# Kernel optimization log

Measured on AMD Instinct MI355X. Metric: run time of the kernel, lower is better.

The kernel has to match this reference:

```python
import jax, jax.numpy as jnp
import numpy as np

K, B, T, Y, X, HY, HX = 8, 64, 128, 128, 64, 256, 256


def sparsemax(z):
    # projection onto the simplex along last axis
    zs = jnp.flip(jnp.sort(z, axis=-1), axis=-1)
    k = jnp.arange(1, z.shape[-1] + 1, dtype=z.dtype)
    cssv = jnp.cumsum(zs, axis=-1) - 1.0
    cond = k * zs > cssv
    kz = jnp.sum(cond, axis=-1, keepdims=True)
    tau = jnp.take_along_axis(cssv, kz - 1, axis=-1) / kz.astype(z.dtype)
    return jnp.maximum(z - tau, 0.0)


def rnn_relu(x, Wih, Whh, bih, bhh, h0):
    # batch-first relu RNN: x [B,T,D] -> h [B,T,H]
    xW = jnp.einsum('btd,hd->bth', x, Wih) + bih
    h0b = jnp.broadcast_to(h0, (x.shape[0], h0.shape[0]))
    def step(h, xt):
        h = jax.nn.relu(xt + h @ Whh.T + bhh)
        return h, h
    _, hs = jax.lax.scan(step, h0b, jnp.swapaxes(xW, 0, 1))
    return jnp.swapaxes(hs, 0, 1)


def setup_inputs() -> dict:
    ks = jax.random.split(jax.random.key(0), 32)
    s = 0.05
    p = lambda k, sh: jax.random.normal(k, sh, jnp.float32) * s
    return {
        'data': jax.random.normal(ks[0], (B, T, Y), jnp.float32),
        'eps_qx': jax.random.normal(ks[1], (K, B, T, X), jnp.float32),
        'eps_z': jax.random.normal(ks[2], (T, B, K), jnp.float32),
        'eps_x': jax.random.normal(ks[3], (T, B, X), jnp.float32),
        'y_Wih': p(ks[4], (K, HY, Y)), 'y_Whh': p(ks[5], (K, HY, HY)),
        'y_bih': p(ks[6], (K, HY)), 'y_bhh': p(ks[7], (K, HY)),
        'y_h0': jnp.zeros((K, HY), jnp.float32),
        'y_Wmu': p(ks[8], (K, X, HY)), 'y_bmu': p(ks[9], (K, X)),
        'x_Wih': p(ks[10], (K, HX, X)), 'x_Whh': p(ks[11], (K, HX, HX)),
        'x_bih': p(ks[12], (K, HX)), 'x_bhh': p(ks[13], (K, HX)),
        'x_h0': jnp.zeros((K, HX), jnp.float32),
        'ds_W': p(ks[14], (HX, K * HX)), 'ds_b': p(ks[15], (HX,)),
        'cb_W1': p(ks[16], (HX, K)), 'cb_b1': p(ks[17], (HX,)),
        'cb_W2': p(ks[18], (K, HX)), 'cb_b2': p(ks[19], (K,)),
        'z_q0': jnp.zeros((K,), jnp.float32),
    }


def _forward(data, eps_qx, eps_z, eps_x, y_Wih, y_Whh, y_bih, y_bhh, y_h0,
             y_Wmu, y_bmu, x_Wih, x_Whh, x_bih, x_bhh, x_h0,
             ds_W, ds_b, cb_W1, cb_b1, cb_W2, cb_b2, z_q0):
    Bn, Tn, _ = data.shape
    Kn = z_q0.shape[0]
    vr = jax.vmap(rnn_relu, in_axes=(None, 0, 0, 0, 0, 0))
    vrx = jax.vmap(rnn_relu, in_axes=(0, 0, 0, 0, 0, 0))
    # per-state LDM inference over reversed y: q(x^k_{1:T} | y_{1:T})
    data_rev = jnp.flip(data, axis=1)
    h_y = jnp.flip(vr(data_rev, y_Wih, y_Whh, y_bih, y_bhh, y_h0), axis=2)  # [K,B,T,HY]
    q_x_mu = jnp.einsum('kbth,kxh->kbtx', h_y, y_Wmu) + y_bmu[:, None, None, :]
    q_x_logvar = jnp.zeros_like(q_x_mu)
    q_x = q_x_mu + eps_qx  # sigma = exp(0.5*0) = 1
    # per-state summary RNN over reversed q_x samples
    q_x_rev = jnp.flip(q_x, axis=2)
    h_x = jnp.flip(vrx(q_x_rev, x_Wih, x_Whh, x_bih, x_bhh, x_h0), axis=2)  # [K,B,T,HX]
    summary = jnp.transpose(h_x, (1, 2, 0, 3)).reshape(Bn, Tn, -1)  # [B,T,K*HX]
    xs = summary @ ds_W.T + ds_b  # downsampler -> [B,T,HX]
    xs_t_all = jnp.swapaxes(xs, 0, 1)              # [T,B,HX]
    mu_t_all = jnp.transpose(q_x_mu, (2, 1, 0, 3))  # [T,B,K,X]
    z0 = jnp.broadcast_to(z_q0, (Bn, Kn))
    def step(z_prev, inp):
        xs_t, mu_t, ez, ex = inp
        h = z_prev @ cb_W1.T + cb_b1 + xs_t          # combiner hidden
        z_mu = h @ cb_W2.T + cb_b2                   # logits mu (logvar=0)
        z_t = z_mu + ez
        w = sparsemax(z_t)                            # [B,K] gating
        x_t = jnp.einsum('bk,bkx->bx', w, mu_t) + ex  # mixture reparam (sigma=1)
        return z_t, (x_t, z_t, z_mu)
    _, (x_s, z_s, z_l) = jax.lax.scan(step, z0, (xs_t_all, mu_t_all, eps_z, eps_x))
    x_sample = jnp.swapaxes(x_s, 0, 1)
    z_sample = jnp.swapaxes(z_s, 0, 1)
    z_logits = jnp.swapaxes(z_l, 0, 1)
    return (x_sample, q_x_mu, q_x_logvar, z_sample, z_logits)


def reference(data, eps_qx, eps_z, eps_x, y_Wih, y_Whh, y_bih, y_bhh, y_h0,
              y_Wmu, y_bmu, x_Wih, x_Whh, x_bih, x_bhh, x_h0,
              ds_W, ds_b, cb_W1, cb_b1, cb_W2, cb_b2, z_q0):
    return _forward(data, eps_qx, eps_z, eps_x, y_Wih, y_Whh, y_bih, y_bhh, y_h0,
                    y_Wmu, y_bmu, x_Wih, x_Whh, x_bih, x_bhh, x_h0,
                    ds_W, ds_b, cb_W1, cb_b1, cb_W2, cb_b2, z_q0)
```

## Files before the change

kernel.cpp:

```cpp
#include <hip/hip_runtime.h>

#define Kc 8
#define Bc 64
#define Tc 128
#define Yc 128
#define Xc 64
#define Hc 256
#define Rc 8192

typedef unsigned short u16;
typedef unsigned int u32;
typedef __attribute__((ext_vector_type(8))) short short8;
typedef __attribute__((ext_vector_type(4))) float f32x4;
typedef __attribute__((ext_vector_type(2))) unsigned int u32x2;

#define OFF_DATA 0L
#define OFF_YWIH 1048576L
#define OFF_YWHH 1310720L
#define OFF_YWMU 1835008L
#define OFF_XWIH 1966080L
#define OFF_XWHH 2097152L
#define OFF_M2   2621440L
#define OFF_QXF  2654208L
#define OFF_BUF1 6848512L
#define U16_BYTES 80805888L
#define FO_YB 0L
#define FO_XB 2048L
#define FO_CB 4096L
#define FO_A2 4112L
#define FO_CP 8192L
#define FO_C  532480L
#define FO_W  598016L


#define O_XS  0L
#define O_QMU 524288L
#define O_QLV 4718592L
#define O_ZS  8912896L
#define O_ZL  8978432L

__device__ __forceinline__ u16 f2bf(float f) {
  union { float f; u32 u; } v; v.f = f;
  u32 u = v.u;
  return (u16)((u + 0x7FFFu + ((u >> 16) & 1u)) >> 16);
}
__device__ __forceinline__ float bitsf(u32 u) {
  union { u32 u; float f; } v; v.u = u; return v.f;
}
__device__ __forceinline__ u32 cvt_pk(float lo, float hi) {
  u32 r;
  asm("v_cvt_pk_bf16_f32 %0, %1, %2" : "=v"(r) : "v"(lo), "v"(hi));
  return r;
}
__device__ __forceinline__ f32x4 mfma16(short8 a, short8 b, f32x4 c) {
  return __builtin_amdgcn_mfma_f32_16x16x32_bf16(a, b, c, 0, 0, 0);
}

__global__ void k_prep(const float* __restrict__ data, const float* __restrict__ yWih,
                       const float* __restrict__ yWhh, const float* __restrict__ yWmu,
                       const float* __restrict__ xWih, const float* __restrict__ xWhh,
                       const float* __restrict__ ybih, const float* __restrict__ ybhh,
                       const float* __restrict__ xbih, const float* __restrict__ xbhh,
                       u16* __restrict__ W, float* __restrict__ F, float* __restrict__ out)
{
  long tid = (long)blockIdx.x * blockDim.x + threadIdx.x;
  long stride = (long)gridDim.x * blockDim.x;
  for (long i = tid; i < 1048576L; i += stride) W[OFF_DATA + i] = f2bf(data[i]);
  for (long i = tid; i < 262144L;  i += stride) W[OFF_YWIH + i] = f2bf(yWih[i]);
  for (long i = tid; i < 524288L;  i += stride) W[OFF_YWHH + i] = f2bf(yWhh[i]);
  for (long i = tid; i < 131072L;  i += stride) W[OFF_YWMU + i] = f2bf(yWmu[i]);
  for (long i = tid; i < 131072L;  i += stride) W[OFF_XWIH + i] = f2bf(xWih[i]);
  for (long i = tid; i < 524288L;  i += stride) W[OFF_XWHH + i] = f2bf(xWhh[i]);
  for (long i = tid; i < 2048L;    i += stride) F[FO_YB + i] = ybih[i] + ybhh[i];
  for (long i = tid; i < 2048L;    i += stride) F[FO_XB + i] = xbih[i] + xbhh[i];
  for (long i = tid; i < 4194304L; i += stride) out[O_QLV + i] = 0.0f;
}

__global__ void k_prep2(const float* __restrict__ dsW, const float* __restrict__ dsb,
                        const float* __restrict__ W1, const float* __restrict__ b1,
                        const float* __restrict__ W2, const float* __restrict__ b2,
                        u16* __restrict__ W, float* __restrict__ F)
{
  if (blockIdx.x < 128) {
    long i = (long)blockIdx.x * 256 + threadIdx.x;
    int k2 = (int)(i >> 11), ki = (int)(i & 2047);
    float s = 0.0f;
    if (k2 < 8) {
      for (int j = 0; j < 256; ++j) s += W2[k2 * 256 + j] * dsW[(long)j * 2048 + ki];
    }
    W[OFF_M2 + i] = f2bf(s);
  } else {
    int t = threadIdx.x;
    if (t < 64) {
      int k2 = t >> 3, k1 = t & 7;
      float s = 0.0f;
      for (int j = 0; j < 256; ++j) s += W2[k2 * 256 + j] * W1[j * 8 + k1];
      F[FO_A2 + t] = s;
    } else if (t < 80) {
      int k2 = t - 64;
      float s = 0.0f;
      if (k2 < 8) {
        for (int j = 0; j < 256; ++j) s += W2[k2 * 256 + j] * (dsb[j] + b1[j]);
        s += b2[k2];
      }
      F[FO_CB + k2] = s;
    }
  }
}

__global__ __launch_bounds__(256) void k_g1(const u16* __restrict__ W, const float* __restrict__ F,
                                            u16* __restrict__ buf)
{
  const int k = blockIdx.y, bs = blockIdx.x >> 5, t0 = (blockIdx.x & 31) * 4;
  const int tid = threadIdx.x, wv = tid >> 6, l = tid & 63, lr = l & 15, lk = l >> 4;
  const int b0 = bs * 16;
  short8 Af[4][4];
  const u16* Ak = W + OFF_YWIH + (long)k * 32768;
#pragma unroll
  for (int nt = 0; nt < 4; ++nt)
#pragma unroll
    for (int kk = 0; kk < 4; ++kk)
      Af[nt][kk] = *(const short8*)(Ak + (long)(wv * 64 + nt * 16 + lr) * 128 + kk * 32 + lk * 8);
  f32x4 bias[4];
#pragma unroll
  for (int nt = 0; nt < 4; ++nt)
    bias[nt] = *(const f32x4*)&F[FO_YB + k * 256 + wv * 64 + nt * 16 + lk * 4];
  int roff[4];
#pragma unroll
  for (int nt = 0; nt < 4; ++nt)
    roff[nt] = (wv * 2 + (nt >> 1)) * 512 + ((nt & 1) * 2 + (lk >> 1)) * 128 + lr * 8 + (lk & 1) * 4;

  for (int ti = 0; ti < 4; ++ti) {
    int t = t0 + ti;
    f32x4 acc[4] = {bias[0], bias[1], bias[2], bias[3]};
    const u16* Brow = W + OFF_DATA + ((long)(b0 + lr) * 128 + t) * 128 + lk * 8;
#pragma unroll
    for (int kk = 0; kk < 4; ++kk) {
      short8 b = *(const short8*)(Brow + kk * 32);
      acc[0] = mfma16(Af[0][kk], b, acc[0]);
      acc[1] = mfma16(Af[1][kk], b, acc[1]);
      acc[2] = mfma16(Af[2][kk], b, acc[2]);
      acc[3] = mfma16(Af[3][kk], b, acc[3]);
    }
    u16* tb = buf + ((long)(k * 4 + bs) * 128 + t) * 4096;
#pragma unroll
    for (int nt = 0; nt < 4; ++nt) {
      u32 d0 = cvt_pk(acc[nt][0], acc[nt][1]);
      u32 d1 = cvt_pk(acc[nt][2], acc[nt][3]);
      *(u32x2*)(tb + roff[nt]) = (u32x2){d0, d1};
    }
  }
}

#define RNNY_STEP(T_, XW_, PIN_, POUT_)                                       \
  {                                                                           \
    f32x4 acc0, acc1;                                                         \
    { u32 w0 = XW_[0], w1 = XW_[1];                                           \
      acc0[0] = bitsf(w0 << 16); acc0[1] = bitsf(w0 & 0xffff0000u);           \
      acc0[2] = bitsf(w1 << 16); acc0[3] = bitsf(w1 & 0xffff0000u); }         \
    { u32 w0 = XW_[2], w1 = XW_[3];                                           \
      acc1[0] = bitsf(w0 << 16); acc1[1] = bitsf(w0 & 0xffff0000u);           \
      acc1[2] = bitsf(w1 << 16); acc1[3] = bitsf(w1 & 0xffff0000u); }         \
    if ((T_) >= 2) {                                                          \
      u32x2 v0 = *(const u32x2*)(tb0 + (long)((T_) - 2) * 4096 + roff[0]);    \
      u32x2 v1 = *(const u32x2*)(tb0 + (long)((T_) - 2) * 4096 + roff[1]);    \
      XW_[0] = v0.x; XW_[1] = v0.y; XW_[2] = v1.x; XW_[3] = v1.y;             \
    }                                                                         \
    _Pragma("unroll")                                                         \
    for (int kk = 0; kk < 8; ++kk) {                                          \
      short8 b = *(const short8*)&hlds[PIN_][kk * 512 + fro];                 \
      acc0 = mfma16(Bf[0][kk], b, acc0);                                      \
      acc1 = mfma16(Bf[1][kk], b, acc1);                                      \
    }                                                                         \
    u16* tb = tb0 + (long)(T_) * 4096;                                        \
    { u32x2 d = (u32x2){cvt_pk(fmaxf(acc0[0], 0.f), fmaxf(acc0[1], 0.f)),     \
                        cvt_pk(fmaxf(acc0[2], 0.f), fmaxf(acc0[3], 0.f))};    \
      *(u32x2*)&hlds[POUT_][roff[0]] = d; *(u32x2*)(tb + roff[0]) = d; }      \
    { u32x2 d = (u32x2){cvt_pk(fmaxf(acc1[0], 0.f), fmaxf(acc1[1], 0.f)),     \
                        cvt_pk(fmaxf(acc1[2], 0.f), fmaxf(acc1[3], 0.f))};    \
      *(u32x2*)&hlds[POUT_][roff[1]] = d; *(u32x2*)(tb + roff[1]) = d; }      \
    asm volatile("s_waitcnt lgkmcnt(0)" ::: "memory");                        \
    __builtin_amdgcn_s_barrier();                                             \
    __builtin_amdgcn_sched_barrier(0);                                        \
  }

__global__ __launch_bounds__(512, 1) void k_rnnY(u16* __restrict__ buf,
                                                 const u16* __restrict__ Whh,
                                                 const float* __restrict__ h0)
{
  const int k = blockIdx.y, bs = blockIdx.x;
  const int tid = threadIdx.x, wv = tid >> 6, l = tid & 63, lr = l & 15, lk = l >> 4;
  const int fro = lk * 128 + lr * 8;
  __shared__ __align__(16) u16 hlds[2][4096];

  short8 Bf[2][8];
  const u16* Wk = Whh + (long)k * 65536;
#pragma unroll
  for (int nt = 0; nt < 2; ++nt)
#pragma unroll
    for (int kk = 0; kk < 8; ++kk)
      Bf[nt][kk] = *(const short8*)(Wk + (long)(wv * 32 + nt * 16 + lr) * 256 + kk * 32 + lk * 8);

  for (int i = tid; i < 4096; i += 512) {
    int n = (i >> 9) * 32 + ((i >> 7) & 3) * 8 + (i & 7);
    hlds[0][i] = f2bf(h0[k * 256 + n]);
  }

  u16* tb0 = buf + (long)(k * 4 + bs) * 128 * 4096;
  int roff[2];
#pragma unroll
  for (int nt = 0; nt < 2; ++nt)
    roff[nt] = wv * 512 + (nt * 2 + (lk >> 1)) * 128 + lr * 8 + (lk & 1) * 4;

  u32 xwA[4], xwB[4];
  {
    u32x2 a0 = *(const u32x2*)(tb0 + (long)(Tc - 1) * 4096 + roff[0]);
    u32x2 a1 = *(const u32x2*)(tb0 + (long)(Tc - 1) * 4096 + roff[1]);
    xwA[0] = a0.x; xwA[1] = a0.y; xwA[2] = a1.x; xwA[3] = a1.y;
    u32x2 b0v = *(const u32x2*)(tb0 + (long)(Tc - 2) * 4096 + roff[0]);
    u32x2 b1v = *(const u32x2*)(tb0 + (long)(Tc - 2) * 4096 + roff[1]);
    xwB[0] = b0v.x; xwB[1] = b0v.y; xwB[2] = b1v.x; xwB[3] = b1v.y;
  }
  __syncthreads();

  for (int t = Tc - 1; t >= 1; t -= 2) {
    RNNY_STEP(t, xwA, 0, 1);
    RNNY_STEP(t - 1, xwB, 1, 0);
  }
}

__global__ __launch_bounds__(256) void k_g2(const u16* __restrict__ W, const u16* __restrict__ hy,
                                            const float* __restrict__ bmu, const float* __restrict__ eps,
                                            float* __restrict__ out, u16* __restrict__ qxf)
{
  const int k = blockIdx.y, bs = blockIdx.x >> 5, t0 = (blockIdx.x & 31) * 4;
  const int tid = threadIdx.x, wv = tid >> 6, l = tid & 63, lr = l & 15, lk = l >> 4;
  const int b0 = bs * 16, x0 = wv * 16;
  short8 Af[8];
  const u16* Ak = W + OFF_YWMU + (long)k * 16384;
#pragma unroll
  for (int kk = 0; kk < 8; ++kk)
    Af[kk] = *(const short8*)(Ak + (long)(x0 + lr) * 256 + kk * 32 + lk * 8);
  f32x4 bias = *(const f32x4*)&bmu[k * 64 + x0 + lk * 4];
  const int qoff = (wv >> 1) * 512 + ((wv & 1) * 2 + (lk >> 1)) * 128 + lr * 8 + (lk & 1) * 4;

  for (int ti = 0; ti < 4; ++ti) {
    int t = t0 + ti;
    const u16* tb = hy + ((long)(k * 4 + bs) * 128 + t) * 4096 + lk * 128 + lr * 8;
    f32x4 a0 = bias, a1 = (f32x4){0.f, 0.f, 0.f, 0.f};
#pragma unroll
    for (int kk = 0; kk < 8; kk += 2) {
      short8 bA = *(const short8*)(tb + kk * 512);
      short8 bB = *(const short8*)(tb + (kk + 1) * 512);
      a0 = mfma16(Af[kk], bA, a0);
      a1 = mfma16(Af[kk + 1], bB, a1);
    }
    f32x4 mu = a0 + a1;
    long idx = ((long)k * Rc + (b0 + lr) * 128 + t) * 64 + x0 + lk * 4;
    *(f32x4*)&out[O_QMU + idx] = mu;
    f32x4 e = *(const f32x4*)&eps[idx];
    f32x4 q = mu + e;
    *(u32x2*)(qxf + ((long)(k * 4 + bs) * 128 + t) * 1024 + qoff) =
        (u32x2){cvt_pk(q[0], q[1]), cvt_pk(q[2], q[3])};
  }
}

#define RNNX_STEP(T_, QC_, PIN_, POUT_)                                       \
  {                                                                           \
    short8 q0 = QC_[0], q1 = QC_[1];                                          \
    if ((T_) >= 2) {                                                          \
      QC_[0] = *(const short8*)(qb0 + (long)((T_) - 2) * 1024 + fro);         \
      QC_[1] = *(const short8*)(qb0 + (long)((T_) - 2) * 1024 + 512 + fro);   \
    }                                                                         \
    f32x4 acc0 = xbias[0], acc1 = xbias[1];                                   \
    f32x4 cacc = (f32x4){0.f, 0.f, 0.f, 0.f};                                 \
    _Pragma("unroll")                                                         \
    for (int kk = 0; kk < 8; ++kk) {                                          \
      short8 b = *(const short8*)&hlds[PIN_][kk * 512 + fro];                 \
      acc0 = mfma16(Bf[0][kk], b, acc0);                                      \
      acc1 = mfma16(Bf[1][kk], b, acc1);                                      \
      if (wv == 0) cacc = mfma16(Mf[kk], b, cacc);                            \
    }                                                                         \
    acc0 = mfma16(IhX[0][0], q0, acc0);                                       \
    acc1 = mfma16(IhX[1][0], q0, acc1);                                       \
    acc0 = mfma16(IhX[0][1], q1, acc0);                                       \
    acc1 = mfma16(IhX[1][1], q1, acc1);                                       \
    if (wv == 0 && (T_) < Tc - 1 && lk < 2)                                   \
      *(f32x4*)&cp[((long)(b0 + lr) * Tc + (T_) + 1) * 8 + lk * 4] = cacc;    \
    { u32x2 d = (u32x2){cvt_pk(fmaxf(acc0[0], 0.f), fmaxf(acc0[1], 0.f)),     \
                        cvt_pk(fmaxf(acc0[2], 0.f), fmaxf(acc0[3], 0.f))};    \
      *(u32x2*)&hlds[POUT_][roff[0]] = d; }                                   \
    { u32x2 d = (u32x2){cvt_pk(fmaxf(acc1[0], 0.f), fmaxf(acc1[1], 0.f)),     \
                        cvt_pk(fmaxf(acc1[2], 0.f), fmaxf(acc1[3], 0.f))};    \
      *(u32x2*)&hlds[POUT_][roff[1]] = d; }                                   \
    asm volatile("s_waitcnt lgkmcnt(0)" ::: "memory");                        \
    __builtin_amdgcn_s_barrier();                                             \
    __builtin_amdgcn_sched_barrier(0);                                        \
  }

__global__ __launch_bounds__(512, 1) void k_rnnX(const u16* __restrict__ W,
                                                 const float* __restrict__ F,
                                                 const u16* __restrict__ qxf,
                                                 const float* __restrict__ h0,
                                                 float* __restrict__ cpart)
{
  const int k = blockIdx.y, bs = blockIdx.x, b0 = bs * 16;
  const int tid = threadIdx.x, wv = tid >> 6, l = tid & 63, lr = l & 15, lk = l >> 4;
  const int fro = lk * 128 + lr * 8;
  __shared__ __align__(16) u16 hlds[2][4096];

  short8 Bf[2][8];
  short8 IhX[2][2];
  short8 Mf[8];
  {
    const u16* Wk = W + OFF_XWHH + (long)k * 65536;
    const u16* Ik = W + OFF_XWIH + (long)k * 16384;
    const u16* Mk = W + OFF_M2 + (long)k * 256;
#pragma unroll
    for (int nt = 0; nt < 2; ++nt) {
#pragma unroll
      for (int kk = 0; kk < 8; ++kk)
        Bf[nt][kk] = *(const short8*)(Wk + (long)(wv * 32 + nt * 16 + lr) * 256 + kk * 32 + lk * 8);
#pragma unroll
      for (int kk = 0; kk < 2; ++kk)
        IhX[nt][kk] = *(const short8*)(Ik + (long)(wv * 32 + nt * 16 + lr) * 64 + kk * 32 + lk * 8);
    }
#pragma unroll
    for (int kk = 0; kk < 8; ++kk)
      Mf[kk] = *(const short8*)(Mk + (long)lr * 2048 + kk * 32 + lk * 8);
  }
  f32x4 xbias[2];
#pragma unroll
  for (int nt = 0; nt < 2; ++nt)
    xbias[nt] = *(const f32x4*)&F[FO_XB + k * 256 + wv * 32 + nt * 16 + lk * 4];
  int roff[2];
#pragma unroll
  for (int nt = 0; nt < 2; ++nt)
    roff[nt] = wv * 512 + (nt * 2 + (lk >> 1)) * 128 + lr * 8 + (lk & 1) * 4;

  for (int i = tid; i < 4096; i += 512) {
    int n = (i >> 9) * 32 + ((i >> 7) & 3) * 8 + (i & 7);
    hlds[0][i] = f2bf(h0[k * 256 + n]);
  }

  const u16* qb0 = qxf + (long)(k * 4 + bs) * 128 * 1024;
  float* cp = cpart + (long)k * Rc * 8;

  short8 qA[2], qB[2];
#pragma unroll
  for (int kk = 0; kk < 2; ++kk) {
    qA[kk] = *(const short8*)(qb0 + (long)(Tc - 1) * 1024 + kk * 512 + fro);
    qB[kk] = *(const short8*)(qb0 + (long)(Tc - 2) * 1024 + kk * 512 + fro);
  }
  __syncthreads();

  for (int t = Tc - 1; t >= 1; t -= 2) {
    RNNX_STEP(t, qA, 0, 1);
    RNNX_STEP(t - 1, qB, 1, 0);
  }
  if (wv == 0) {
    f32x4 cacc = (f32x4){0.f, 0.f, 0.f, 0.f};
#pragma unroll
    for (int kk = 0; kk < 8; ++kk) {
      short8 b = *(const short8*)&hlds[0][kk * 512 + fro];
      cacc = mfma16(Mf[kk], b, cacc);
    }
    if (lk < 2)
      *(f32x4*)&cp[((long)(b0 + lr) * Tc) * 8 + lk * 4] = cacc;
  }
}

__global__ void k_csum(const float* __restrict__ cpart, const float* __restrict__ F,
                       float* __restrict__ cbuf)
{
  int i = blockIdx.x * 256 + threadIdx.x;
  float s = F[FO_CB + (i & 7)];
#pragma unroll
  for (int k = 0; k < 8; ++k) s += cpart[(long)k * 65536 + i];
  cbuf[i] = s;
}

#define CASD(a, b) { float _hi = fmaxf(a, b), _lo = fminf(a, b); a = _hi; b = _lo; }
__global__ __launch_bounds__(256) void k_zchain(const float* __restrict__ F, const float* __restrict__ cbuf,
                                                const float* __restrict__ eps_z, const float* __restrict__ zq0,
                                                float* __restrict__ out, float* __restrict__ wbuf)
{
  const int wv = threadIdx.x >> 6, l = threadIdx.x & 63;
  const int b = blockIdx.x * 4 + wv;
  __shared__ float cl[4][1024];
  __shared__ float el[4][1024];
  for (int i = l; i < 1024; i += 64) cl[wv][i] = cbuf[(long)b * 1024 + i];
  for (int i = l; i < 1024; i += 64) {
    int t = i >> 3, kk = i & 7;
    el[wv][i] = eps_z[(long)t * (Bc * Kc) + b * 8 + kk];
  }
  float a2 = F[FO_A2 + l];
  __syncthreads();

  float z = zq0[l & 7];
  for (int t = 0; t < Tc; ++t) {
    float p = a2 * z;
    p += __shfl_xor(p, 1, 64);
    p += __shfl_xor(p, 2, 64);
    p += __shfl_xor(p, 4, 64);
    float zmu_l = __shfl(p, (l & 7) * 8, 64);
    float zl = zmu_l + cl[wv][t * 8 + (l & 7)];
    float zt = zl + el[wv][t * 8 + (l & 7)];

    float v0 = __shfl(zt, 0, 64), v1 = __shfl(zt, 1, 64), v2 = __shfl(zt, 2, 64), v3 = __shfl(zt, 3, 64);
    float v4 = __shfl(zt, 4, 64), v5 = __shfl(zt, 5, 64), v6 = __shfl(zt, 6, 64), v7 = __shfl(zt, 7, 64);
    CASD(v0, v1); CASD(v2, v3); CASD(v4, v5); CASD(v6, v7);
    CASD(v0, v2); CASD(v1, v3); CASD(v4, v6); CASD(v5, v7);
    CASD(v1, v2); CASD(v5, v6);
    CASD(v0, v4); CASD(v1, v5); CASD(v2, v6); CASD(v3, v7);
    CASD(v2, v4); CASD(v3, v5);
    CASD(v1, v2); CASD(v3, v4); CASD(v5, v6);
    float s0 = v0, s1 = s0 + v1, s2 = s1 + v2, s3 = s2 + v3;
    float s4 = s3 + v4, s5 = s4 + v5, s6 = s5 + v6, s7 = s6 + v7;
    int kz = 1;
    kz += (2.0f * v1 > s1 - 1.0f) ? 1 : 0;
    kz += (3.0f * v2 > s2 - 1.0f) ? 1 : 0;
    kz += (4.0f * v3 > s3 - 1.0f) ? 1 : 0;
    kz += (5.0f * v4 > s4 - 1.0f) ? 1 : 0;
    kz += (6.0f * v5 > s5 - 1.0f) ? 1 : 0;
    kz += (7.0f * v6 > s6 - 1.0f) ? 1 : 0;
    kz += (8.0f * v7 > s7 - 1.0f) ? 1 : 0;
    float csel = s0 - 1.0f;
    csel = (kz > 1) ? s1 - 1.0f : csel;
    csel = (kz > 2) ? s2 - 1.0f : csel;
    csel = (kz > 3) ? s3 - 1.0f : csel;
    csel = (kz > 4) ? s4 - 1.0f : csel;
    csel = (kz > 5) ? s5 - 1.0f : csel;
    csel = (kz > 6) ? s6 - 1.0f : csel;
    csel = (kz > 7) ? s7 - 1.0f : csel;
    float tau = csel / (float)kz;
    float wk = fmaxf(zt - tau, 0.0f);

    if (l < 8) {
      long r = (long)b * Tc + t;
      out[O_ZL + r * 8 + l] = zl;
      out[O_ZS + r * 8 + l] = zt;
      wbuf[r * 8 + l] = wk;
    }
    z = zt;
  }
}

__global__ void k_xsample(const float* __restrict__ wbuf, const float* __restrict__ eps_x,
                          float* __restrict__ out)
{
  long idx = (long)blockIdx.x * 256 + threadIdx.x;
  if (idx >= (long)Rc * Xc) return;
  long r = idx >> 6;
  int x = (int)(idx & 63);
  long b = r >> 7;
  long t = r & 127;
  float s = eps_x[(t * Bc + b) * 64 + x];
#pragma unroll
  for (int k = 0; k < 8; ++k)
    s += wbuf[r * 8 + k] * out[O_QMU + ((long)k * Rc + r) * 64 + x];
  out[O_XS + idx] = s;
}

extern "C" void kernel_launch(void* const* d_in, const int* in_sizes, int n_in,
                              void* d_out, int out_size, void* d_ws, size_t ws_size,
                              hipStream_t stream) {
  (void)in_sizes; (void)n_in; (void)out_size; (void)ws_size;
  const float* data   = (const float*)d_in[0];
  const float* eps_qx = (const float*)d_in[1];
  const float* eps_z  = (const float*)d_in[2];
  const float* eps_x  = (const float*)d_in[3];
  const float* yWih   = (const float*)d_in[4];
  const float* yWhh   = (const float*)d_in[5];
  const float* ybih   = (const float*)d_in[6];
  const float* ybhh   = (const float*)d_in[7];
  const float* yh0    = (const float*)d_in[8];
  const float* yWmu   = (const float*)d_in[9];
  const float* ybmu   = (const float*)d_in[10];
  const float* xWih   = (const float*)d_in[11];
  const float* xWhh   = (const float*)d_in[12];
  const float* xbih   = (const float*)d_in[13];
  const float* xbhh   = (const float*)d_in[14];
  const float* xh0    = (const float*)d_in[15];
  const float* dsW    = (const float*)d_in[16];
  const float* dsb    = (const float*)d_in[17];
  const float* cbW1   = (const float*)d_in[18];
  const float* cbb1   = (const float*)d_in[19];
  const float* cbW2   = (const float*)d_in[20];
  const float* cbb2   = (const float*)d_in[21];
  const float* zq0    = (const float*)d_in[22];

  u16*   W = (u16*)d_ws;
  float* F = (float*)((char*)d_ws + U16_BYTES);
  float* out = (float*)d_out;

  hipLaunchKernelGGL(k_prep, dim3(1024), dim3(256), 0, stream,
                     data, yWih, yWhh, yWmu, xWih, xWhh, ybih, ybhh, xbih, xbhh, W, F, out);
  hipLaunchKernelGGL(k_prep2, dim3(129), dim3(256), 0, stream,
                     dsW, dsb, cbW1, cbb1, cbW2, cbb2, W, F);
  hipLaunchKernelGGL(k_g1, dim3(128, 8), dim3(256), 0, stream, W, F, W + OFF_BUF1);
  hipLaunchKernelGGL(k_rnnY, dim3(4, 8), dim3(512), 0, stream, W + OFF_BUF1, W + OFF_YWHH, yh0);
  hipLaunchKernelGGL(k_g2, dim3(128, 8), dim3(256), 0, stream,
                     W, W + OFF_BUF1, ybmu, eps_qx, out, W + OFF_QXF);
  hipLaunchKernelGGL(k_rnnX, dim3(4, 8), dim3(512), 0, stream,
                     W, F, W + OFF_QXF, xh0, F + FO_CP);
  hipLaunchKernelGGL(k_csum, dim3(256), dim3(256), 0, stream, F + FO_CP, F, F + FO_C);
  hipLaunchKernelGGL(k_zchain, dim3(16), dim3(256), 0, stream, F, F + FO_C, eps_z, zq0, out, F + FO_W);
  hipLaunchKernelGGL(k_xsample, dim3(2048), dim3(256), 0, stream, F + FO_W, eps_x, out);
}
```

Before: 288.4 us.

## Run z-chain with one thread per batch row and register-held state

Rewrites the sequential sparsemax z-chain so each of 64 threads owns one batch element and keeps the 8x8 combiner matrix and the 8 logits in registers. This removes the per-step cross-lane shuffle reductions and the LDS staging. Per-step cbuf and eps_z values are prefetched two steps ahead with vector loads, and outputs are written as float4. The grid shrinks to a single 64-thread block, so the serial chain now runs on one CU with heavier per-thread work and higher register pressure.

```diff
diff --git a/kernel.cpp b/kernel.cpp
--- a/kernel.cpp
+++ b/kernel.cpp
@@ -380,69 +380,94 @@
   cbuf[i] = s;
 }
 
-#define CASD(a, b) { float _hi = fmaxf(a, b), _lo = fminf(a, b); a = _hi; b = _lo; }
-__global__ __launch_bounds__(256) void k_zchain(const float* __restrict__ F, const float* __restrict__ cbuf,
-                                                const float* __restrict__ eps_z, const float* __restrict__ zq0,
-                                                float* __restrict__ out, float* __restrict__ wbuf)
-{
-  const int wv = threadIdx.x >> 6, l = threadIdx.x & 63;
-  const int b = blockIdx.x * 4 + wv;
-  __shared__ float cl[4][1024];
-  __shared__ float el[4][1024];
-  for (int i = l; i < 1024; i += 64) cl[wv][i] = cbuf[(long)b * 1024 + i];
-  for (int i = l; i < 1024; i += 64) {
-    int t = i >> 3, kk = i & 7;
-    el[wv][i] = eps_z[(long)t * (Bc * Kc) + b * 8 + kk];
-  }
-  float a2 = F[FO_A2 + l];
-  __syncthreads();
-
-  float z = zq0[l & 7];
-  for (int t = 0; t < Tc; ++t) {
-    float p = a2 * z;
-    p += __shfl_xor(p, 1, 64);
-    p += __shfl_xor(p, 2, 64);
-    p += __shfl_xor(p, 4, 64);
-    float zmu_l = __shfl(p, (l & 7) * 8, 64);
-    float zl = zmu_l + cl[wv][t * 8 + (l & 7)];
-    float zt = zl + el[wv][t * 8 + (l & 7)];
-
-    float v0 = __shfl(zt, 0, 64), v1 = __shfl(zt, 1, 64), v2 = __shfl(zt, 2, 64), v3 = __shfl(zt, 3, 64);
-    float v4 = __shfl(zt, 4, 64), v5 = __shfl(zt, 5, 64), v6 = __shfl(zt, 6, 64), v7 = __shfl(zt, 7, 64);
-    CASD(v0, v1); CASD(v2, v3); CASD(v4, v5); CASD(v6, v7);
-    CASD(v0, v2); CASD(v1, v3); CASD(v4, v6); CASD(v5, v7);
-    CASD(v1, v2); CASD(v5, v6);
-    CASD(v0, v4); CASD(v1, v5); CASD(v2, v6); CASD(v3, v7);
-    CASD(v2, v4); CASD(v3, v5);
-    CASD(v1, v2); CASD(v3, v4); CASD(v5, v6);
-    float s0 = v0, s1 = s0 + v1, s2 = s1 + v2, s3 = s2 + v3;
-    float s4 = s3 + v4, s5 = s4 + v5, s6 = s5 + v6, s7 = s6 + v7;
-    int kz = 1;
-    kz += (2.0f * v1 > s1 - 1.0f) ? 1 : 0;
-    kz += (3.0f * v2 > s2 - 1.0f) ? 1 : 0;
-    kz += (4.0f * v3 > s3 - 1.0f) ? 1 : 0;
-    kz += (5.0f * v4 > s4 - 1.0f) ? 1 : 0;
-    kz += (6.0f * v5 > s5 - 1.0f) ? 1 : 0;
-    kz += (7.0f * v6 > s6 - 1.0f) ? 1 : 0;
-    kz += (8.0f * v7 > s7 - 1.0f) ? 1 : 0;
-    float csel = s0 - 1.0f;
-    csel = (kz > 1) ? s1 - 1.0f : csel;
-    csel = (kz > 2) ? s2 - 1.0f : csel;
-    csel = (kz > 3) ? s3 - 1.0f : csel;
-    csel = (kz > 4) ? s4 - 1.0f : csel;
-    csel = (kz > 5) ? s5 - 1.0f : csel;
-    csel = (kz > 6) ? s6 - 1.0f : csel;
-    csel = (kz > 7) ? s7 - 1.0f : csel;
-    float tau = csel / (float)kz;
-    float wk = fmaxf(zt - tau, 0.0f);
-
-    if (l < 8) {
-      long r = (long)b * Tc + t;
-      out[O_ZL + r * 8 + l] = zl;
-      out[O_ZS + r * 8 + l] = zt;
-      wbuf[r * 8 + l] = wk;
-    }
-    z = zt;
+#define CASS(a, b) { float _hi = fmaxf(a, b), _lo = fminf(a, b); a = _hi; b = _lo; }
+#define ZSTEP(T_, C0_, C1_, E0_, E1_)                                          \
+  {                                                                            \
+    float c_[8] = {C0_[0], C0_[1], C0_[2], C0_[3], C1_[0], C1_[1], C1_[2], C1_[3]}; \
+    float e_[8] = {E0_[0], E0_[1], E0_[2], E0_[3], E1_[0], E1_[1], E1_[2], E1_[3]}; \
+    if ((T_) + 2 < Tc) {                                                       \
+      C0_ = *(const f32x4*)&cbuf[(long)b * 1024 + ((T_) + 2) * 8];             \
+      C1_ = *(const f32x4*)&cbuf[(long)b * 1024 + ((T_) + 2) * 8 + 4];         \
+      E0_ = *(const f32x4*)&eps_z[(long)((T_) + 2) * 512 + b * 8];             \
+      E1_ = *(const f32x4*)&eps_z[(long)((T_) + 2) * 512 + b * 8 + 4];         \
+    }                                                                          \
+    float zl_[8], zt_[8];                                                      \
+    _Pragma("unroll")                                                          \
+    for (int j = 0; j < 8; ++j) {                                              \
+      float s_ = 0.0f;                                                         \
+      _Pragma("unroll")                                                        \
+      for (int q_ = 0; q_ < 8; ++q_) s_ = fmaf(A2r[j * 8 + q_], z[q_], s_);    \
+      zl_[j] = s_ + c_[j];                                                     \
+      zt_[j] = zl_[j] + e_[j];                                                 \
+    }                                                                          \
+    long rbase = ((long)b * Tc + (T_)) * 8;                                    \
+    *(f32x4*)&out[O_ZL + rbase]     = (f32x4){zl_[0], zl_[1], zl_[2], zl_[3]}; \
+    *(f32x4*)&out[O_ZL + rbase + 4] = (f32x4){zl_[4], zl_[5], zl_[6], zl_[7]}; \
+    *(f32x4*)&out[O_ZS + rbase]     = (f32x4){zt_[0], zt_[1], zt_[2], zt_[3]}; \
+    *(f32x4*)&out[O_ZS + rbase + 4] = (f32x4){zt_[4], zt_[5], zt_[6], zt_[7]}; \
+    float v0 = zt_[0], v1 = zt_[1], v2 = zt_[2], v3 = zt_[3];                  \
+    float v4 = zt_[4], v5 = zt_[5], v6 = zt_[6], v7 = zt_[7];                  \
+    CASS(v0, v1); CASS(v2, v3); CASS(v4, v5); CASS(v6, v7);                    \
+    CASS(v0, v2); CASS(v1, v3); CASS(v4, v6); CASS(v5, v7);                    \
+    CASS(v1, v2); CASS(v5, v6);                                                \
+    CASS(v0, v4); CASS(v1, v5); CASS(v2, v6); CASS(v3, v7);                    \
+    CASS(v2, v4); CASS(v3, v5);                                                \
+    CASS(v1, v2); CASS(v3, v4); CASS(v5, v6);                                  \
+    float s0 = v0, s1 = s0 + v1, s2 = s1 + v2, s3 = s2 + v3;                   \
+    float s4 = s3 + v4, s5 = s4 + v5, s6 = s5 + v6, s7 = s6 + v7;              \
+    int kz = 1;                                                                \
+    kz += (2.0f * v1 > s1 - 1.0f) ? 1 : 0;                                     \
+    kz += (3.0f * v2 > s2 - 1.0f) ? 1 : 0;                                     \
+    kz += (4.0f * v3 > s3 - 1.0f) ? 1 : 0;                                     \
+    kz += (5.0f * v4 > s4 - 1.0f) ? 1 : 0;                                     \
+    kz += (6.0f * v5 > s5 - 1.0f) ? 1 : 0;                                     \
+    kz += (7.0f * v6 > s6 - 1.0f) ? 1 : 0;                                     \
+    kz += (8.0f * v7 > s7 - 1.0f) ? 1 : 0;                                     \
+    float csel = s0 - 1.0f;                                                    \
+    csel = (kz > 1) ? s1 - 1.0f : csel;                                        \
+    csel = (kz > 2) ? s2 - 1.0f : csel;                                        \
+    csel = (kz > 3) ? s3 - 1.0f : csel;                                        \
+    csel = (kz > 4) ? s4 - 1.0f : csel;                                        \
+    csel = (kz > 5) ? s5 - 1.0f : csel;                                        \
+    csel = (kz > 6) ? s6 - 1.0f : csel;                                        \
+    csel = (kz > 7) ? s7 - 1.0f : csel;                                        \
+    float tau = csel / (float)kz;                                              \
+    float w_[8];                                                               \
+    _Pragma("unroll")                                                          \
+    for (int j = 0; j < 8; ++j) w_[j] = fmaxf(zt_[j] - tau, 0.0f);             \
+    *(f32x4*)&wbuf[rbase]     = (f32x4){w_[0], w_[1], w_[2], w_[3]};           \
+    *(f32x4*)&wbuf[rbase + 4] = (f32x4){w_[4], w_[5], w_[6], w_[7]};           \
+    _Pragma("unroll")                                                          \
+    for (int j = 0; j < 8; ++j) z[j] = zt_[j];                                 \
+  }
+
+__global__ __launch_bounds__(64) void k_zchain(const float* __restrict__ F,
+                                               const float* __restrict__ cbuf,
+                                               const float* __restrict__ eps_z,
+                                               const float* __restrict__ zq0,
+                                               float* __restrict__ out,
+                                               float* __restrict__ wbuf)
+{
+  const int b = threadIdx.x;
+  float A2r[64];
+#pragma unroll
+  for (int i = 0; i < 64; ++i) A2r[i] = F[FO_A2 + i];
+  float z[8];
+#pragma unroll
+  for (int j = 0; j < 8; ++j) z[j] = zq0[j];
+
+  f32x4 cA0 = *(const f32x4*)&cbuf[(long)b * 1024 + 0];
+  f32x4 cA1 = *(const f32x4*)&cbuf[(long)b * 1024 + 4];
+  f32x4 eA0 = *(const f32x4*)&eps_z[(long)0 * 512 + b * 8];
+  f32x4 eA1 = *(const f32x4*)&eps_z[(long)0 * 512 + b * 8 + 4];
+  f32x4 cB0 = *(const f32x4*)&cbuf[(long)b * 1024 + 8];
+  f32x4 cB1 = *(const f32x4*)&cbuf[(long)b * 1024 + 12];
+  f32x4 eB0 = *(const f32x4*)&eps_z[(long)1 * 512 + b * 8];
+  f32x4 eB1 = *(const f32x4*)&eps_z[(long)1 * 512 + b * 8 + 4];
+
+  for (int t = 0; t < Tc; t += 2) {
+    ZSTEP(t, cA0, cA1, eA0, eA1);
+    ZSTEP(t + 1, cB0, cB1, eB0, eB1);
   }
 }
 
@@ -505,6 +530,6 @@
   hipLaunchKernelGGL(k_rnnX, dim3(4, 8), dim3(512), 0, stream,
                      W, F, W + OFF_QXF, xh0, F + FO_CP);
   hipLaunchKernelGGL(k_csum, dim3(256), dim3(256), 0, stream, F + FO_CP, F, F + FO_C);
-  hipLaunchKernelGGL(k_zchain, dim3(16), dim3(256), 0, stream, F, F + FO_C, eps_z, zq0, out, F + FO_W);
+  hipLaunchKernelGGL(k_zchain, dim3(1), dim3(64), 0, stream, F, F + FO_C, eps_z, zq0, out, F + FO_W);
   hipLaunchKernelGGL(k_xsample, dim3(2048), dim3(256), 0, stream, F + FO_W, eps_x, out);
 }
```

Result: slower. 294.5 us (+2.1%).
